# Kernel tuning notes

Measured on AMD Instinct MI355X. Metric: run time of the kernel, lower is better.

Reference implementation:

```python
import jax, jax.numpy as jnp
import numpy as np

NUM_HEADS = 16
HEIGHT = 32
WIDTH = 32
FEATURES_DIM = HEIGHT * WIDTH  # 1024
EMBED_DIM = 1024


def setup_inputs() -> dict:
    key = jax.random.key(0)
    ks = jax.random.split(key, 9)
    s_in = 1.0 / np.sqrt(FEATURES_DIM)
    s_e = 1.0 / np.sqrt(EMBED_DIM)
    return {
        "x": jax.random.normal(ks[0], (16, 512, HEIGHT, WIDTH), dtype=jnp.float32),
        "Wq": jax.random.uniform(ks[1], (EMBED_DIM, FEATURES_DIM), jnp.float32, -s_in, s_in),
        "bq": jax.random.uniform(ks[2], (EMBED_DIM,), jnp.float32, -s_in, s_in),
        "Wk": jax.random.uniform(ks[3], (EMBED_DIM, FEATURES_DIM), jnp.float32, -s_in, s_in),
        "bk": jax.random.uniform(ks[4], (EMBED_DIM,), jnp.float32, -s_in, s_in),
        "Wv": jax.random.uniform(ks[5], (EMBED_DIM, FEATURES_DIM), jnp.float32, -s_in, s_in),
        "bv": jax.random.uniform(ks[6], (EMBED_DIM,), jnp.float32, -s_in, s_in),
        "Wo": jax.random.uniform(ks[7], (FEATURES_DIM, EMBED_DIM), jnp.float32, -s_e, s_e),
        "bo": jax.random.uniform(ks[8], (FEATURES_DIM,), jnp.float32, -s_e, s_e),
    }


def reference(x, Wq, bq, Wk, bk, Wv, bv, Wo, bo):
    B, C, H, W = x.shape
    nh = NUM_HEADS
    hd = EMBED_DIM // nh
    xf = x.reshape(B, C, H * W)  # [B, C, F] - channel tokens
    q = xf @ Wq.T + bq  # [B, C, E]
    k = xf @ Wk.T + bk
    v = xf @ Wv.T + bv
    q = q.reshape(B, C, nh, hd).transpose(0, 2, 1, 3)  # [B, nh, C, hd]
    k = k.reshape(B, C, nh, hd).transpose(0, 2, 1, 3)
    v = v.reshape(B, C, nh, hd).transpose(0, 2, 1, 3)
    scores = jnp.einsum("bhcd,bhkd->bhck", q, k) / jnp.sqrt(jnp.float32(hd))
    attn = jax.nn.softmax(scores, axis=-1)
    out = jnp.einsum("bhck,bhkd->bhcd", attn, v)  # [B, nh, C, hd]
    out = out.transpose(0, 2, 1, 3).reshape(B, C, EMBED_DIM)
    out = out @ Wo.T + bo  # [B, C, F]
    return out.reshape(B, C, H, W)
```

## Files before the change

kernel.cpp:

```cpp
#include <hip/hip_runtime.h>


typedef unsigned short u16;
typedef __attribute__((ext_vector_type(8))) short short8;
typedef __attribute__((ext_vector_type(4))) float f32x4;
typedef __attribute__((ext_vector_type(4))) unsigned short u16x4;

#define MFMA16(a, b, c) __builtin_amdgcn_mfma_f32_16x16x32_bf16(a, b, c, 0, 0, 0)

__device__ __forceinline__ u16 f2bf(float x) {
  unsigned u = __float_as_uint(x);
  u += 0x7FFFu + ((u >> 16) & 1u);
  return (u16)(u >> 16);
}

__device__ __forceinline__ void async16(const void* g, void* l) {
  __builtin_amdgcn_global_load_lds(
      (__attribute__((address_space(1))) unsigned int*)(g),
      (__attribute__((address_space(3))) unsigned int*)(l), 16, 0, 0);
}

__global__ __launch_bounds__(256) void cvt_all(
    const float* __restrict__ x, const float* __restrict__ wq,
    const float* __restrict__ wk, const float* __restrict__ wv,
    const float* __restrict__ wo, u16* __restrict__ dst) {
  int g = blockIdx.x * 256 + threadIdx.x;
  const float* s;
  int off;
  if (g < 2097152) {
    s = x; off = g;
  } else {
    int r = g - 2097152;
    int w = r >> 18;
    off = r & 262143;
    s = (w == 0) ? wq : (w == 1) ? wk : (w == 2) ? wv : wo;
  }
  f32x4 v = ((const f32x4*)s)[off];
  u16x4 o;
#pragma unroll
  for (int j = 0; j < 4; ++j) o[j] = f2bf(v[j]);
  ((u16x4*)dst)[g] = o;
}

__device__ __forceinline__ void gemm8p(const u16* __restrict__ A,
                                       const u16* __restrict__ W, int m0,
                                       int n0, u16* lds, f32x4 acc[8][4]) {
  const int t = threadIdx.x;
  const int wave = t >> 6, lane = t & 63, lr = lane & 15, lg = lane >> 4;
  const int wr = wave >> 2, wn = wave & 3;
  const int srow = t >> 3;
  const int scol = ((t & 7) ^ (srow & 7)) << 3;
  const u16* gA = A + (size_t)(m0 + srow) * 1024 + scol;
  const u16* gB = W + (size_t)(n0 + srow) * 1024 + scol;
  u16* stA = lds + wave * 512;
  u16* stB = lds + 16384 + wave * 512;
  const int arow = (wr * 128 + lr) * 64;
  const int brow = 16384 + (wn * 64 + lr) * 64;
  const int xk = lr & 7;
  const int sw0 = (lg ^ xk) << 3;
  const int sw1 = ((4 + lg) ^ xk) << 3;

#define SA(kt, h)                                                           \
  {                                                                         \
    async16(gA + (2 * (h)) * 65536 + (kt) * 64,                             \
            stA + ((kt) & 1) * 32768 + (2 * (h)) * 4096);                   \
    async16(gA + (2 * (h) + 1) * 65536 + (kt) * 64,                         \
            stA + ((kt) & 1) * 32768 + (2 * (h) + 1) * 4096);               \
  }
#define SB(kt, h)                                                           \
  {                                                                         \
    async16(gB + (2 * (h)) * 65536 + (kt) * 64,                             \
            stB + ((kt) & 1) * 32768 + (2 * (h)) * 4096);                   \
    async16(gB + (2 * (h) + 1) * 65536 + (kt) * 64,                         \
            stB + ((kt) & 1) * 32768 + (2 * (h) + 1) * 4096);               \
  }

  SB(0, 0); SA(0, 0); SB(0, 1); SA(0, 1);
  SB(1, 0); SA(1, 0);
  asm volatile("s_waitcnt vmcnt(4)" ::: "memory");
  __builtin_amdgcn_s_barrier();

  short8 a[8], b[8];
#pragma unroll 2
  for (int tt = 0; tt < 16; ++tt) {
    const u16* bp = lds + (tt & 1) * 32768;
#pragma unroll
    for (int mf = 0; mf < 4; ++mf) {
      a[mf * 2 + 0] = *(const short8*)(bp + arow + mf * 1024 + sw0);
      a[mf * 2 + 1] = *(const short8*)(bp + arow + mf * 1024 + sw1);
    }
#pragma unroll
    for (int nf = 0; nf < 2; ++nf) {
      b[nf * 2 + 0] = *(const short8*)(bp + brow + nf * 1024 + sw0);
      b[nf * 2 + 1] = *(const short8*)(bp + brow + nf * 1024 + sw1);
    }
    if (tt + 1 < 16) SB(tt + 1, 1);
    __builtin_amdgcn_s_barrier();
    asm volatile("s_waitcnt lgkmcnt(0)" ::: "memory");
    __builtin_amdgcn_sched_barrier(0);
    __builtin_amdgcn_s_setprio(1);
#pragma unroll
    for (int mf = 0; mf < 4; ++mf)
#pragma unroll
      for (int nf = 0; nf < 2; ++nf) {
        acc[mf][nf] = MFMA16(a[mf * 2 + 0], b[nf * 2 + 0], acc[mf][nf]);
        acc[mf][nf] = MFMA16(a[mf * 2 + 1], b[nf * 2 + 1], acc[mf][nf]);
      }
    __builtin_amdgcn_s_setprio(0);
    __builtin_amdgcn_s_barrier();
#pragma unroll
    for (int nf = 2; nf < 4; ++nf) {
      b[nf * 2 + 0] = *(const short8*)(bp + brow + nf * 1024 + sw0);
      b[nf * 2 + 1] = *(const short8*)(bp + brow + nf * 1024 + sw1);
    }
    if (tt + 1 < 16) SA(tt + 1, 1);
    __builtin_amdgcn_s_barrier();
    asm volatile("s_waitcnt lgkmcnt(0)" ::: "memory");
    __builtin_amdgcn_sched_barrier(0);
    __builtin_amdgcn_s_setprio(1);
#pragma unroll
    for (int mf = 0; mf < 4; ++mf)
#pragma unroll
      for (int nf = 2; nf < 4; ++nf) {
        acc[mf][nf] = MFMA16(a[mf * 2 + 0], b[nf * 2 + 0], acc[mf][nf]);
        acc[mf][nf] = MFMA16(a[mf * 2 + 1], b[nf * 2 + 1], acc[mf][nf]);
      }
    __builtin_amdgcn_s_setprio(0);
    __builtin_amdgcn_s_barrier();
#pragma unroll
    for (int mf = 4; mf < 8; ++mf) {
      a[(mf - 4) * 2 + 0] = *(const short8*)(bp + arow + mf * 1024 + sw0);
      a[(mf - 4) * 2 + 1] = *(const short8*)(bp + arow + mf * 1024 + sw1);
    }
    if (tt + 2 < 16) SB(tt + 2, 0);
    __builtin_amdgcn_s_barrier();
    asm volatile("s_waitcnt lgkmcnt(0)" ::: "memory");
    __builtin_amdgcn_sched_barrier(0);
    __builtin_amdgcn_s_setprio(1);
#pragma unroll
    for (int mf = 4; mf < 8; ++mf)
#pragma unroll
      for (int nf = 2; nf < 4; ++nf) {
        acc[mf][nf] = MFMA16(a[(mf - 4) * 2 + 0], b[nf * 2 + 0], acc[mf][nf]);
        acc[mf][nf] = MFMA16(a[(mf - 4) * 2 + 1], b[nf * 2 + 1], acc[mf][nf]);
      }
    __builtin_amdgcn_s_setprio(0);
    __builtin_amdgcn_s_barrier();
    if (tt + 2 < 16) SA(tt + 2, 0);
    __builtin_amdgcn_s_setprio(1);
#pragma unroll
    for (int mf = 4; mf < 8; ++mf)
#pragma unroll
      for (int nf = 0; nf < 2; ++nf) {
        acc[mf][nf] = MFMA16(a[(mf - 4) * 2 + 0], b[nf * 2 + 0], acc[mf][nf]);
        acc[mf][nf] = MFMA16(a[(mf - 4) * 2 + 1], b[nf * 2 + 1], acc[mf][nf]);
      }
    __builtin_amdgcn_s_setprio(0);
    if (tt < 14) {
      asm volatile("s_waitcnt vmcnt(4)" ::: "memory");
    } else {
      asm volatile("s_waitcnt vmcnt(0)" ::: "memory");
    }
    __builtin_amdgcn_s_barrier();
  }
#undef SA
#undef SB
}

__device__ __forceinline__ void gemm2x(const u16* __restrict__ A,
                                       const u16* __restrict__ W, int m0,
                                       int n0, u16* lds, f32x4 acc[8][2]) {
  const int t = threadIdx.x;
  const int wave = t >> 6, lane = t & 63, lr = lane & 15, lg = lane >> 4;
  const int wr = wave >> 2, wn = wave & 3;
  const int srow = t >> 3;
  const int scol = ((t & 7) ^ (srow & 7)) << 3;
  const u16* gA = A + (size_t)(m0 + srow) * 1024 + scol;
  const u16* gB = W + (size_t)(n0 + srow) * 1024 + scol;
  u16* stA = lds + wave * 512;
  u16* stB = lds + 16384 + wave * 512;
  const int arow = (wr * 128 + lr) * 64;
  const int brow = 16384 + (wn * 32 + lr) * 64;
  const int xk = lr & 7;
  const int sw0 = (lg ^ xk) << 3;
  const int sw1 = ((4 + lg) ^ xk) << 3;

#define SA2(kt)                                                              \
  {                                                                          \
    async16(gA + 0 * 65536 + (kt) * 64, stA + ((kt) & 1) * 24576 + 0 * 4096); \
    async16(gA + 1 * 65536 + (kt) * 64, stA + ((kt) & 1) * 24576 + 1 * 4096); \
    async16(gA + 2 * 65536 + (kt) * 64, stA + ((kt) & 1) * 24576 + 2 * 4096); \
    async16(gA + 3 * 65536 + (kt) * 64, stA + ((kt) & 1) * 24576 + 3 * 4096); \
  }
#define SB2(kt)                                                              \
  {                                                                          \
    async16(gB + 0 * 65536 + (kt) * 64, stB + ((kt) & 1) * 24576 + 0 * 4096); \
    async16(gB + 1 * 65536 + (kt) * 64, stB + ((kt) & 1) * 24576 + 1 * 4096); \
  }

  SA2(0); SB2(0);
  asm volatile("s_waitcnt vmcnt(0)" ::: "memory");
  __builtin_amdgcn_s_barrier();

  short8 a[8], b[4];
#pragma unroll 2
  for (int tt = 0; tt < 16; ++tt) {
    const u16* bp = lds + (tt & 1) * 24576;
#pragma unroll
    for (int mf = 0; mf < 4; ++mf) {
      a[mf * 2 + 0] = *(const short8*)(bp + arow + mf * 1024 + sw0);
      a[mf * 2 + 1] = *(const short8*)(bp + arow + mf * 1024 + sw1);
    }
#pragma unroll
    for (int nf = 0; nf < 2; ++nf) {
      b[nf * 2 + 0] = *(const short8*)(bp + brow + nf * 1024 + sw0);
      b[nf * 2 + 1] = *(const short8*)(bp + brow + nf * 1024 + sw1);
    }
    if (tt + 1 < 16) { SA2(tt + 1); SB2(tt + 1); }
    __builtin_amdgcn_s_barrier();
    asm volatile("s_waitcnt lgkmcnt(0)" ::: "memory");
    __builtin_amdgcn_sched_barrier(0);
    __builtin_amdgcn_s_setprio(1);
#pragma unroll
    for (int mf = 0; mf < 4; ++mf)
#pragma unroll
      for (int nf = 0; nf < 2; ++nf) {
        acc[mf][nf] = MFMA16(a[mf * 2 + 0], b[nf * 2 + 0], acc[mf][nf]);
        acc[mf][nf] = MFMA16(a[mf * 2 + 1], b[nf * 2 + 1], acc[mf][nf]);
      }
    __builtin_amdgcn_s_setprio(0);
    __builtin_amdgcn_s_barrier();
#pragma unroll
    for (int mf = 4; mf < 8; ++mf) {
      a[(mf - 4) * 2 + 0] = *(const short8*)(bp + arow + mf * 1024 + sw0);
      a[(mf - 4) * 2 + 1] = *(const short8*)(bp + arow + mf * 1024 + sw1);
    }
    __builtin_amdgcn_s_barrier();
    asm volatile("s_waitcnt lgkmcnt(0)" ::: "memory");
    __builtin_amdgcn_sched_barrier(0);
    __builtin_amdgcn_s_setprio(1);
#pragma unroll
    for (int mf = 4; mf < 8; ++mf)
#pragma unroll
      for (int nf = 0; nf < 2; ++nf) {
        acc[mf][nf] = MFMA16(a[(mf - 4) * 2 + 0], b[nf * 2 + 0], acc[mf][nf]);
        acc[mf][nf] = MFMA16(a[(mf - 4) * 2 + 1], b[nf * 2 + 1], acc[mf][nf]);
      }
    __builtin_amdgcn_s_setprio(0);
    asm volatile("s_waitcnt vmcnt(0)" ::: "memory");
    __builtin_amdgcn_s_barrier();
  }
#undef SA2
#undef SB2
}

__global__ __launch_bounds__(512, 2) void gemm_qkv(
    const u16* __restrict__ xb, const u16* __restrict__ w3,
    const float* __restrict__ bq, const float* __restrict__ bk,
    const float* __restrict__ bv, u16* __restrict__ qo, u16* __restrict__ ko,
    u16* __restrict__ vo) {
  __shared__ u16 lds[65536];
  const int id = blockIdx.x;
  const int lid = (id & 7) * 48 + (id >> 3);
  const int tm = lid / 12, tn = lid % 12;
  const int m0 = tm * 256, n0g = tn * 256;
  const int z = n0g >> 10, n0 = n0g & 1023;
  const float* bias = (z == 0) ? bq : (z == 1) ? bk : bv;
  u16* outp = (z == 0) ? qo : (z == 1) ? ko : vo;
  f32x4 acc[8][4];
#pragma unroll
  for (int i = 0; i < 8; ++i)
#pragma unroll
    for (int j = 0; j < 4; ++j) acc[i][j] = (f32x4){0.f, 0.f, 0.f, 0.f};
  gemm8p(xb, w3, m0, n0g, lds, acc);

  const int t = threadIdx.x;
  const int wave = t >> 6, lane = t & 63, lr = lane & 15, lg = lane >> 4;
  const int wr = wave >> 2, wn = wave & 3;
  float bb[4];
#pragma unroll
  for (int nf = 0; nf < 4; ++nf) bb[nf] = bias[n0 + wn * 64 + nf * 16 + lr];
#pragma unroll
  for (int mf = 0; mf < 8; ++mf)
#pragma unroll
    for (int nf = 0; nf < 4; ++nf)
#pragma unroll
      for (int r = 0; r < 4; ++r) {
        int m = m0 + wr * 128 + mf * 16 + lg * 4 + r;
        int n = n0 + wn * 64 + nf * 16 + lr;
        float val = acc[mf][nf][r] + bb[nf];
        int b_ = m >> 9, c = m & 511, h = n >> 6, dd = n & 63;
        int idx = (z == 2) ? ((((b_ << 4) + h) << 15) + (dd << 9) + c)
                           : ((((b_ << 4) + h) << 15) + (c << 6) + dd);
        outp[idx] = f2bf(val);
      }
}

__global__ __launch_bounds__(512, 1) void gemm_oproj(const u16* __restrict__ ab,
                                                     const u16* __restrict__ wo,
                                                     const float* __restrict__ bo,
                                                     float* __restrict__ out) {
  __shared__ u16 lds[49152];
  const int id = blockIdx.x;
  const int lid = (id & 7) * 32 + (id >> 3);
  const int m0 = (lid >> 3) * 256, n0 = (lid & 7) * 128;
  f32x4 acc[8][2];
#pragma unroll
  for (int i = 0; i < 8; ++i)
#pragma unroll
    for (int j = 0; j < 2; ++j) acc[i][j] = (f32x4){0.f, 0.f, 0.f, 0.f};
  gemm2x(ab, wo, m0, n0, lds, acc);

  const int t = threadIdx.x;
  const int wave = t >> 6, lane = t & 63, lr = lane & 15, lg = lane >> 4;
  const int wr = wave >> 2, wn = wave & 3;
  float bb[2];
#pragma unroll
  for (int nf = 0; nf < 2; ++nf) bb[nf] = bo[n0 + wn * 32 + nf * 16 + lr];
#pragma unroll
  for (int mf = 0; mf < 8; ++mf)
#pragma unroll
    for (int nf = 0; nf < 2; ++nf)
#pragma unroll
      for (int r = 0; r < 4; ++r) {
        int m = m0 + wr * 128 + mf * 16 + lg * 4 + r;
        int n = n0 + wn * 32 + nf * 16 + lr;
        out[m * 1024 + n] = acc[mf][nf][r] + bb[nf];
      }
}

__global__ __launch_bounds__(512, 2) void attn_kernel(
    const u16* __restrict__ qb, const u16* __restrict__ kb,
    const u16* __restrict__ vb, u16* __restrict__ ab) {
  __shared__ u16 lK[32768];
  __shared__ u16 lV[32768];
  __shared__ u16 lP[8192];
  const int t = threadIdx.x;
  const int bh = blockIdx.x;
  const int b_ = bh >> 4, h_ = bh & 15;
  const u16* kg = kb + bh * 32768;
  const u16* vg = vb + bh * 32768;
#pragma unroll
  for (int i = 0; i < 8; ++i) {
    int row = i * 64 + (t >> 3), slot = t & 7;
    short8 kv = *(const short8*)(kg + row * 64 + slot * 8);
    *(short8*)(lK + row * 64 + ((slot ^ (row & 7)) << 3)) = kv;
    int vrow = i * 8 + (t >> 6), vslot = t & 63;
    short8 vv = *(const short8*)(vg + vrow * 512 + vslot * 8);
    *(short8*)(lV + vrow * 512 + ((vslot ^ (vrow & 7)) << 3)) = vv;
  }
  __syncthreads();

  const int wv_ = t >> 6, lane = t & 63, lr = lane & 15, lg = lane >> 4;
  u16* lPw = lP + wv_ * 1024;
  const u16* qg = qb + bh * 32768;
  const float sc = 0.125f * 1.44269504088896f;

#pragma unroll 1
  for (int qi = 0; qi < 4; ++qi) {
    const int qrow = (wv_ * 4 + qi) * 16;
    short8 a0 = *(const short8*)(qg + (qrow + lr) * 64 + lg * 8);
    short8 a1 = *(const short8*)(qg + (qrow + lr) * 64 + 32 + lg * 8);
    f32x4 s[32];
#pragma unroll
    for (int f = 0; f < 32; ++f) {
      const u16* kr = lK + (f * 16 + lr) * 64;
      short8 k0 = *(const short8*)(kr + ((lg ^ (lr & 7)) << 3));
      short8 k1 = *(const short8*)(kr + (((4 + lg) ^ (lr & 7)) << 3));
      f32x4 z4 = (f32x4){0.f, 0.f, 0.f, 0.f};
      z4 = MFMA16(a0, k0, z4);
      z4 = MFMA16(a1, k1, z4);
      s[f] = z4;
    }
    float inv[4];
#pragma unroll
    for (int r = 0; r < 4; ++r) {
      float m_ = s[0][r];
#pragma unroll
      for (int f = 1; f < 32; ++f) m_ = fmaxf(m_, s[f][r]);
      m_ = fmaxf(m_, __shfl_xor(m_, 1));
      m_ = fmaxf(m_, __shfl_xor(m_, 2));
      m_ = fmaxf(m_, __shfl_xor(m_, 4));
      m_ = fmaxf(m_, __shfl_xor(m_, 8));
      float sm = 0.f;
#pragma unroll
      for (int f = 0; f < 32; ++f) {
        float e = exp2f((s[f][r] - m_) * sc);
        s[f][r] = e;
        sm += e;
      }
      sm += __shfl_xor(sm, 1);
      sm += __shfl_xor(sm, 2);
      sm += __shfl_xor(sm, 4);
      sm += __shfl_xor(sm, 8);
      inv[r] = 1.f / sm;
    }
    f32x4 o[4];
#pragma unroll
    for (int i = 0; i < 4; ++i) o[i] = (f32x4){0.f, 0.f, 0.f, 0.f};
#pragma unroll
    for (int ch = 0; ch < 8; ++ch) {
#pragma unroll
      for (int cf = 0; cf < 4; ++cf)
#pragma unroll
        for (int r = 0; r < 4; ++r) {
          int q = lg * 4 + r, kc = cf * 16 + lr;
          lPw[q * 64 + (((kc >> 3) ^ (q & 7)) << 3) + (kc & 7)] =
              f2bf(s[ch * 4 + cf][r]);
        }
      asm volatile("s_waitcnt lgkmcnt(0)" ::: "memory");
      const u16* pr = lPw + lr * 64;
      short8 pa0 = *(const short8*)(pr + ((lg ^ (lr & 7)) << 3));
      short8 pa1 = *(const short8*)(pr + (((4 + lg) ^ (lr & 7)) << 3));
#pragma unroll
      for (int df = 0; df < 4; ++df) {
        const u16* vr = lV + (df * 16 + lr) * 512;
        short8 v0 = *(const short8*)(vr + (((ch * 8 + lg) ^ (lr & 7)) << 3));
        short8 v1 =
            *(const short8*)(vr + (((ch * 8 + 4 + lg) ^ (lr & 7)) << 3));
        o[df] = MFMA16(pa0, v0, o[df]);
        o[df] = MFMA16(pa1, v1, o[df]);
      }
    }
#pragma unroll
    for (int df = 0; df < 4; ++df)
#pragma unroll
      for (int r = 0; r < 4; ++r) {
        int q = qrow + lg * 4 + r, dd = df * 16 + lr;
        ab[(b_ * 512 + q) * 1024 + h_ * 64 + dd] = f2bf(o[df][r] * inv[r]);
      }
  }
}

extern "C" void kernel_launch(void* const* d_in, const int* in_sizes, int n_in,
                              void* d_out, int out_size, void* d_ws,
                              size_t ws_size, hipStream_t stream) {
  (void)in_sizes; (void)n_in; (void)out_size;
  const float* x  = (const float*)d_in[0];
  const float* Wq = (const float*)d_in[1];
  const float* bq = (const float*)d_in[2];
  const float* Wk = (const float*)d_in[3];
  const float* bk = (const float*)d_in[4];
  const float* Wv = (const float*)d_in[5];
  const float* bv = (const float*)d_in[6];
  const float* Wo = (const float*)d_in[7];
  const float* bo = (const float*)d_in[8];
  float* out = (float*)d_out;

  if (ws_size < 75497472u) return;
  u16* xb  = (u16*)d_ws;
  u16* w3b = xb + 8388608;
  u16* wob = w3b + 3145728;
  u16* qbuf = wob + 1048576;
  u16* kbuf = qbuf + 8388608;
  u16* vbuf = kbuf + 8388608;
  u16* abuf = xb;

  cvt_all<<<12288, 256, 0, stream>>>(x, Wq, Wk, Wv, Wo, xb);
  gemm_qkv<<<384, 512, 0, stream>>>(xb, w3b, bq, bk, bv, qbuf, kbuf, vbuf);
  attn_kernel<<<256, 512, 0, stream>>>(qbuf, kbuf, vbuf, abuf);
  gemm_oproj<<<256, 512, 0, stream>>>(abuf, wob, bo, out);
}
```

Measured before the change: 168.2 us.

## Split attention across query quarters with two-pass online softmax over key halves

The attention kernel now launches one block per (batch, head, query quarter), 1024 blocks instead of 256. Each wave handles a single 16-row query tile. Keys and values are streamed in two 256-key halves, and an online-softmax rescale replaces the full-row softmax. This halves LDS use per block and raises the occupancy target so more blocks fit per CU. In exchange, K and V are reloaded once per query quarter (4x global traffic for K/V), and there are extra syncs and rescale work. A block-index swizzle spreads neighbouring blocks across heads.

After: 189.5 us. +12.7%, slower.

```diff
diff --git a/kernel.cpp b/kernel.cpp
--- a/kernel.cpp
+++ b/kernel.cpp
@@ -329,41 +329,55 @@
       }
 }
 
-__global__ __launch_bounds__(512, 2) void attn_kernel(
+__global__ __launch_bounds__(512, 4) void attn_kernel(
     const u16* __restrict__ qb, const u16* __restrict__ kb,
     const u16* __restrict__ vb, u16* __restrict__ ab) {
-  __shared__ u16 lK[32768];
-  __shared__ u16 lV[32768];
+  __shared__ u16 lK[16384];
+  __shared__ u16 lV[16384];
   __shared__ u16 lP[8192];
   const int t = threadIdx.x;
-  const int bh = blockIdx.x;
+  const int id = blockIdx.x;
+  const int bid = (id & 7) * 128 + (id >> 3);
+  const int bh = bid >> 2, qq = bid & 3;
   const int b_ = bh >> 4, h_ = bh & 15;
   const u16* kg = kb + bh * 32768;
   const u16* vg = vb + bh * 32768;
-#pragma unroll
-  for (int i = 0; i < 8; ++i) {
-    int row = i * 64 + (t >> 3), slot = t & 7;
-    short8 kv = *(const short8*)(kg + row * 64 + slot * 8);
-    *(short8*)(lK + row * 64 + ((slot ^ (row & 7)) << 3)) = kv;
-    int vrow = i * 8 + (t >> 6), vslot = t & 63;
-    short8 vv = *(const short8*)(vg + vrow * 512 + vslot * 8);
-    *(short8*)(lV + vrow * 512 + ((vslot ^ (vrow & 7)) << 3)) = vv;
-  }
-  __syncthreads();
-
+  const u16* qg = qb + bh * 32768;
   const int wv_ = t >> 6, lane = t & 63, lr = lane & 15, lg = lane >> 4;
   u16* lPw = lP + wv_ * 1024;
-  const u16* qg = qb + bh * 32768;
   const float sc = 0.125f * 1.44269504088896f;
+  const int qrow = qq * 128 + wv_ * 16;
+
+  short8 a0 = *(const short8*)(qg + (qrow + lr) * 64 + lg * 8);
+  short8 a1 = *(const short8*)(qg + (qrow + lr) * 64 + 32 + lg * 8);
+
+  float m_[4], l_[4];
+  f32x4 o[4];
+#pragma unroll
+  for (int r = 0; r < 4; ++r) { m_[r] = -1e30f; l_[r] = 0.f; }
+#pragma unroll
+  for (int i = 0; i < 4; ++i) o[i] = (f32x4){0.f, 0.f, 0.f, 0.f};
 
 #pragma unroll 1
-  for (int qi = 0; qi < 4; ++qi) {
-    const int qrow = (wv_ * 4 + qi) * 16;
-    short8 a0 = *(const short8*)(qg + (qrow + lr) * 64 + lg * 8);
-    short8 a1 = *(const short8*)(qg + (qrow + lr) * 64 + 32 + lg * 8);
-    f32x4 s[32];
-#pragma unroll
-    for (int f = 0; f < 32; ++f) {
+  for (int kh = 0; kh < 2; ++kh) {
+    __syncthreads();
+#pragma unroll
+    for (int i = 0; i < 4; ++i) {
+      int row = i * 64 + (t >> 3), slot = t & 7;
+      short8 kv = *(const short8*)(kg + (kh * 256 + row) * 64 + slot * 8);
+      *(short8*)(lK + row * 64 + ((slot ^ (row & 7)) << 3)) = kv;
+    }
+#pragma unroll
+    for (int i = 0; i < 4; ++i) {
+      int vrow = i * 16 + (t >> 5), vslot = t & 31;
+      short8 vv = *(const short8*)(vg + vrow * 512 + kh * 256 + vslot * 8);
+      *(short8*)(lV + vrow * 256 + ((vslot ^ (vrow & 7)) << 3)) = vv;
+    }
+    __syncthreads();
+
+    f32x4 s[16];
+#pragma unroll
+    for (int f = 0; f < 16; ++f) {
       const u16* kr = lK + (f * 16 + lr) * 64;
       short8 k0 = *(const short8*)(kr + ((lg ^ (lr & 7)) << 3));
       short8 k1 = *(const short8*)(kr + (((4 + lg) ^ (lr & 7)) << 3));
@@ -372,20 +386,22 @@
       z4 = MFMA16(a1, k1, z4);
       s[f] = z4;
     }
-    float inv[4];
+    float scl[4];
 #pragma unroll
     for (int r = 0; r < 4; ++r) {
-      float m_ = s[0][r];
-#pragma unroll
-      for (int f = 1; f < 32; ++f) m_ = fmaxf(m_, s[f][r]);
-      m_ = fmaxf(m_, __shfl_xor(m_, 1));
-      m_ = fmaxf(m_, __shfl_xor(m_, 2));
-      m_ = fmaxf(m_, __shfl_xor(m_, 4));
-      m_ = fmaxf(m_, __shfl_xor(m_, 8));
+      float pm = s[0][r];
+#pragma unroll
+      for (int f = 1; f < 16; ++f) pm = fmaxf(pm, s[f][r]);
+      pm = fmaxf(pm, __shfl_xor(pm, 1));
+      pm = fmaxf(pm, __shfl_xor(pm, 2));
+      pm = fmaxf(pm, __shfl_xor(pm, 4));
+      pm = fmaxf(pm, __shfl_xor(pm, 8));
+      float mn = fmaxf(m_[r], pm);
+      scl[r] = exp2f((m_[r] - mn) * sc);
       float sm = 0.f;
 #pragma unroll
-      for (int f = 0; f < 32; ++f) {
-        float e = exp2f((s[f][r] - m_) * sc);
+      for (int f = 0; f < 16; ++f) {
+        float e = exp2f((s[f][r] - mn) * sc);
         s[f][r] = e;
         sm += e;
       }
@@ -393,13 +409,15 @@
       sm += __shfl_xor(sm, 2);
       sm += __shfl_xor(sm, 4);
       sm += __shfl_xor(sm, 8);
-      inv[r] = 1.f / sm;
-    }
-    f32x4 o[4];
-#pragma unroll
-    for (int i = 0; i < 4; ++i) o[i] = (f32x4){0.f, 0.f, 0.f, 0.f};
-#pragma unroll
-    for (int ch = 0; ch < 8; ++ch) {
+      l_[r] = l_[r] * scl[r] + sm;
+      m_[r] = mn;
+    }
+#pragma unroll
+    for (int df = 0; df < 4; ++df)
+#pragma unroll
+      for (int r = 0; r < 4; ++r) o[df][r] *= scl[r];
+#pragma unroll
+    for (int ch = 0; ch < 4; ++ch) {
 #pragma unroll
       for (int cf = 0; cf < 4; ++cf)
 #pragma unroll
@@ -414,7 +432,7 @@
       short8 pa1 = *(const short8*)(pr + (((4 + lg) ^ (lr & 7)) << 3));
 #pragma unroll
       for (int df = 0; df < 4; ++df) {
-        const u16* vr = lV + (df * 16 + lr) * 512;
+        const u16* vr = lV + (df * 16 + lr) * 256;
         short8 v0 = *(const short8*)(vr + (((ch * 8 + lg) ^ (lr & 7)) << 3));
         short8 v1 =
             *(const short8*)(vr + (((ch * 8 + 4 + lg) ^ (lr & 7)) << 3));
@@ -422,14 +440,17 @@
         o[df] = MFMA16(pa1, v1, o[df]);
       }
     }
-#pragma unroll
-    for (int df = 0; df < 4; ++df)
-#pragma unroll
-      for (int r = 0; r < 4; ++r) {
-        int q = qrow + lg * 4 + r, dd = df * 16 + lr;
-        ab[(b_ * 512 + q) * 1024 + h_ * 64 + dd] = f2bf(o[df][r] * inv[r]);
-      }
-  }
+  }
+  float inv[4];
+#pragma unroll
+  for (int r = 0; r < 4; ++r) inv[r] = 1.f / l_[r];
+#pragma unroll
+  for (int df = 0; df < 4; ++df)
+#pragma unroll
+    for (int r = 0; r < 4; ++r) {
+      int q = qrow + lg * 4 + r, dd = df * 16 + lr;
+      ab[(b_ * 512 + q) * 1024 + h_ * 64 + dd] = f2bf(o[df][r] * inv[r]);
+    }
 }
 
 extern "C" void kernel_launch(void* const* d_in, const int* in_sizes, int n_in,
@@ -458,6 +479,6 @@
 
   cvt_all<<<12288, 256, 0, stream>>>(x, Wq, Wk, Wv, Wo, xb);
   gemm_qkv<<<384, 512, 0, stream>>>(xb, w3b, bq, bk, bv, qbuf, kbuf, vbuf);
-  attn_kernel<<<256, 512, 0, stream>>>(qbuf, kbuf, vbuf, abuf);
+  attn_kernel<<<1024, 512, 0, stream>>>(qbuf, kbuf, vbuf, abuf);
   gemm_oproj<<<256, 512, 0, stream>>>(abuf, wob, bo, out);
 }
```

## Replace 8-phase interleaved GEMM pipeline with simpler 2-phase K-split schedule

Applied to the files above, without the earlier changes.

The QKV GEMM mainloop drops the 8-phase schedule, which staggered half-tile async loads one and two tiles ahead across four MFMA quadrants. In its place is a 2-phase loop: the whole next K tile is issued at once, each phase computes all 8x4 fragments over one K half, and the loop ends with a full vmcnt(0) wait. This cuts barriers and register pressure (b shrinks from 8 to 4 fragments), but prefetch depth drops to a single tile and each iteration ends with a full global-load drain, which can expose memory latency.

New measurement: 172.1 us. 1.02x slower.

```diff
diff --git a/kernel.cpp b/kernel.cpp
--- a/kernel.cpp
+++ b/kernel.cpp
@@ -42,7 +42,7 @@
   ((u16x4*)dst)[g] = o;
 }
 
-__device__ __forceinline__ void gemm8p(const u16* __restrict__ A,
+__device__ __forceinline__ void gemm2k(const u16* __restrict__ A,
                                        const u16* __restrict__ W, int m0,
                                        int n0, u16* lds, f32x4 acc[8][4]) {
   const int t = threadIdx.x;
@@ -60,111 +60,68 @@
   const int sw0 = (lg ^ xk) << 3;
   const int sw1 = ((4 + lg) ^ xk) << 3;
 
-#define SA(kt, h)                                                           \
-  {                                                                         \
-    async16(gA + (2 * (h)) * 65536 + (kt) * 64,                             \
-            stA + ((kt) & 1) * 32768 + (2 * (h)) * 4096);                   \
-    async16(gA + (2 * (h) + 1) * 65536 + (kt) * 64,                         \
-            stA + ((kt) & 1) * 32768 + (2 * (h) + 1) * 4096);               \
-  }
-#define SB(kt, h)                                                           \
-  {                                                                         \
-    async16(gB + (2 * (h)) * 65536 + (kt) * 64,                             \
-            stB + ((kt) & 1) * 32768 + (2 * (h)) * 4096);                   \
-    async16(gB + (2 * (h) + 1) * 65536 + (kt) * 64,                         \
-            stB + ((kt) & 1) * 32768 + (2 * (h) + 1) * 4096);               \
-  }
-
-  SB(0, 0); SA(0, 0); SB(0, 1); SA(0, 1);
-  SB(1, 0); SA(1, 0);
-  asm volatile("s_waitcnt vmcnt(4)" ::: "memory");
+#define SAll(kt)                                                             \
+  {                                                                          \
+    async16(gA + 0 * 65536 + (kt) * 64, stA + ((kt) & 1) * 32768 + 0 * 4096); \
+    async16(gA + 1 * 65536 + (kt) * 64, stA + ((kt) & 1) * 32768 + 1 * 4096); \
+    async16(gA + 2 * 65536 + (kt) * 64, stA + ((kt) & 1) * 32768 + 2 * 4096); \
+    async16(gA + 3 * 65536 + (kt) * 64, stA + ((kt) & 1) * 32768 + 3 * 4096); \
+  }
+#define SBll(kt)                                                             \
+  {                                                                          \
+    async16(gB + 0 * 65536 + (kt) * 64, stB + ((kt) & 1) * 32768 + 0 * 4096); \
+    async16(gB + 1 * 65536 + (kt) * 64, stB + ((kt) & 1) * 32768 + 1 * 4096); \
+    async16(gB + 2 * 65536 + (kt) * 64, stB + ((kt) & 1) * 32768 + 2 * 4096); \
+    async16(gB + 3 * 65536 + (kt) * 64, stB + ((kt) & 1) * 32768 + 3 * 4096); \
+  }
+
+  SAll(0); SBll(0);
+  asm volatile("s_waitcnt vmcnt(0)" ::: "memory");
   __builtin_amdgcn_s_barrier();
 
-  short8 a[8], b[8];
+  short8 a[8], b[4];
 #pragma unroll 2
   for (int tt = 0; tt < 16; ++tt) {
     const u16* bp = lds + (tt & 1) * 32768;
 #pragma unroll
-    for (int mf = 0; mf < 4; ++mf) {
-      a[mf * 2 + 0] = *(const short8*)(bp + arow + mf * 1024 + sw0);
-      a[mf * 2 + 1] = *(const short8*)(bp + arow + mf * 1024 + sw1);
-    }
-#pragma unroll
-    for (int nf = 0; nf < 2; ++nf) {
-      b[nf * 2 + 0] = *(const short8*)(bp + brow + nf * 1024 + sw0);
-      b[nf * 2 + 1] = *(const short8*)(bp + brow + nf * 1024 + sw1);
-    }
-    if (tt + 1 < 16) SB(tt + 1, 1);
+    for (int mf = 0; mf < 8; ++mf)
+      a[mf] = *(const short8*)(bp + arow + mf * 1024 + sw0);
+#pragma unroll
+    for (int nf = 0; nf < 4; ++nf)
+      b[nf] = *(const short8*)(bp + brow + nf * 1024 + sw0);
+    if (tt + 1 < 16) { SAll(tt + 1); SBll(tt + 1); }
     __builtin_amdgcn_s_barrier();
     asm volatile("s_waitcnt lgkmcnt(0)" ::: "memory");
     __builtin_amdgcn_sched_barrier(0);
     __builtin_amdgcn_s_setprio(1);
 #pragma unroll
-    for (int mf = 0; mf < 4; ++mf)
-#pragma unroll
-      for (int nf = 0; nf < 2; ++nf) {
-        acc[mf][nf] = MFMA16(a[mf * 2 + 0], b[nf * 2 + 0], acc[mf][nf]);
-        acc[mf][nf] = MFMA16(a[mf * 2 + 1], b[nf * 2 + 1], acc[mf][nf]);
-      }
+    for (int mf = 0; mf < 8; ++mf)
+#pragma unroll
+      for (int nf = 0; nf < 4; ++nf)
+        acc[mf][nf] = MFMA16(a[mf], b[nf], acc[mf][nf]);
     __builtin_amdgcn_s_setprio(0);
     __builtin_amdgcn_s_barrier();
 #pragma unroll
-    for (int nf = 2; nf < 4; ++nf) {
-      b[nf * 2 + 0] = *(const short8*)(bp + brow + nf * 1024 + sw0);
-      b[nf * 2 + 1] = *(const short8*)(bp + brow + nf * 1024 + sw1);
-    }
-    if (tt + 1 < 16) SA(tt + 1, 1);
+    for (int mf = 0; mf < 8; ++mf)
+      a[mf] = *(const short8*)(bp + arow + mf * 1024 + sw1);
+#pragma unroll
+    for (int nf = 0; nf < 4; ++nf)
+      b[nf] = *(const short8*)(bp + brow + nf * 1024 + sw1);
     __builtin_amdgcn_s_barrier();
     asm volatile("s_waitcnt lgkmcnt(0)" ::: "memory");
     __builtin_amdgcn_sched_barrier(0);
     __builtin_amdgcn_s_setprio(1);
 #pragma unroll
-    for (int mf = 0; mf < 4; ++mf)
-#pragma unroll
-      for (int nf = 2; nf < 4; ++nf) {
-        acc[mf][nf] = MFMA16(a[mf * 2 + 0], b[nf * 2 + 0], acc[mf][nf]);
-        acc[mf][nf] = MFMA16(a[mf * 2 + 1], b[nf * 2 + 1], acc[mf][nf]);
-      }
+    for (int mf = 0; mf < 8; ++mf)
+#pragma unroll
+      for (int nf = 0; nf < 4; ++nf)
+        acc[mf][nf] = MFMA16(a[mf], b[nf], acc[mf][nf]);
     __builtin_amdgcn_s_setprio(0);
-    __builtin_amdgcn_s_barrier();
-#pragma unroll
-    for (int mf = 4; mf < 8; ++mf) {
-      a[(mf - 4) * 2 + 0] = *(const short8*)(bp + arow + mf * 1024 + sw0);
-      a[(mf - 4) * 2 + 1] = *(const short8*)(bp + arow + mf * 1024 + sw1);
-    }
-    if (tt + 2 < 16) SB(tt + 2, 0);
-    __builtin_amdgcn_s_barrier();
-    asm volatile("s_waitcnt lgkmcnt(0)" ::: "memory");
-    __builtin_amdgcn_sched_barrier(0);
-    __builtin_amdgcn_s_setprio(1);
-#pragma unroll
-    for (int mf = 4; mf < 8; ++mf)
-#pragma unroll
-      for (int nf = 2; nf < 4; ++nf) {
-        acc[mf][nf] = MFMA16(a[(mf - 4) * 2 + 0], b[nf * 2 + 0], acc[mf][nf]);
-        acc[mf][nf] = MFMA16(a[(mf - 4) * 2 + 1], b[nf * 2 + 1], acc[mf][nf]);
-      }
-    __builtin_amdgcn_s_setprio(0);
-    __builtin_amdgcn_s_barrier();
-    if (tt + 2 < 16) SA(tt + 2, 0);
-    __builtin_amdgcn_s_setprio(1);
-#pragma unroll
-    for (int mf = 4; mf < 8; ++mf)
-#pragma unroll
-      for (int nf = 0; nf < 2; ++nf) {
-        acc[mf][nf] = MFMA16(a[(mf - 4) * 2 + 0], b[nf * 2 + 0], acc[mf][nf]);
-        acc[mf][nf] = MFMA16(a[(mf - 4) * 2 + 1], b[nf * 2 + 1], acc[mf][nf]);
-      }
-    __builtin_amdgcn_s_setprio(0);
-    if (tt < 14) {
-      asm volatile("s_waitcnt vmcnt(4)" ::: "memory");
-    } else {
-      asm volatile("s_waitcnt vmcnt(0)" ::: "memory");
-    }
-    __builtin_amdgcn_s_barrier();
-  }
-#undef SA
-#undef SB
+    asm volatile("s_waitcnt vmcnt(0)" ::: "memory");
+    __builtin_amdgcn_s_barrier();
+  }
+#undef SAll
+#undef SBll
 }
 
 __device__ __forceinline__ void gemm2x(const u16* __restrict__ A,
@@ -272,7 +229,7 @@
   for (int i = 0; i < 8; ++i)
 #pragma unroll
     for (int j = 0; j < 4; ++j) acc[i][j] = (f32x4){0.f, 0.f, 0.f, 0.f};
-  gemm8p(xb, w3, m0, n0g, lds, acc);
+  gemm2k(xb, w3, m0, n0g, lds, acc);
 
   const int t = threadIdx.x;
   const int wave = t >> 6, lane = t & 63, lr = lane & 15, lg = lane >> 4;
```
